# Performance work log

Measured on AMD Instinct MI355X. Metric: run time of the kernel, lower is better.

Reference implementation:

```python
import jax, jax.numpy as jnp
import numpy as np

L, N, D = 4, 50000, 64        # lookback, n_nodes, gnn_dim
E = 500000                    # n_edges
HID = 256
LN_EPS = 1e-5


def setup_inputs() -> dict:
    key = jax.random.key(0)
    ks = jax.random.split(key, 8)
    h_all = jax.random.normal(ks[0], (L, N, D), dtype=jnp.float32)
    src = jax.random.randint(ks[1], (E,), 0, N, dtype=jnp.int32)
    dst = jax.random.randint(ks[2], (E,), 0, N, dtype=jnp.int32)
    W1 = jax.random.normal(ks[3], (HID, L * 2 * D), dtype=jnp.float32) * (1.0 / np.sqrt(L * 2 * D))
    b1 = jax.random.normal(ks[4], (HID,), dtype=jnp.float32) * 0.01
    W3 = jax.random.normal(ks[5], (1, HID), dtype=jnp.float32) * (1.0 / np.sqrt(HID))
    b3 = jax.random.normal(ks[6], (1,), dtype=jnp.float32) * 0.01
    gamma2 = jnp.ones((HID,), dtype=jnp.float32)
    beta2 = jnp.zeros((HID,), dtype=jnp.float32)
    return {"h_all": h_all, "src": src, "dst": dst, "W1": W1, "b1": b1,
            "W3": W3, "b3": b3, "gamma2": gamma2, "beta2": beta2}


def reference(h_all, src, dst, W1, b1, W3, b3, gamma2, beta2):
    lb, _, d = h_all.shape
    # importance weights 1..L normalized
    imp = jnp.arange(1, lb + 1, dtype=h_all.dtype)
    imp = imp / imp.sum()
    # per-edge gather of src/dst features for every lookback step: [L, E, 2D]
    hs = h_all[:, src]                                  # [L, E, D]
    hd = h_all[:, dst]                                  # [L, E, D]
    embed = jnp.concatenate([hs, hd], axis=-1) * imp[:, None, None]
    # concat over lookback steps -> [E, L*2D]
    embed = jnp.transpose(embed, (1, 0, 2)).reshape(embed.shape[1], -1)
    # MLP: W1(tanh) -> LayerNorm -> dropout(eval=identity) -> relu -> W3
    x = jnp.tanh(embed) @ W1.T + b1                     # [E, HID]
    mu = jnp.mean(x, axis=-1, keepdims=True)
    var = jnp.var(x, axis=-1, keepdims=True)
    x = (x - mu) * jax.lax.rsqrt(var + LN_EPS) * gamma2 + beta2
    x = jax.nn.relu(x)
    out = x @ W3.T + b3                                 # [E, 1]
    return out[:, 0]
```

## Files before the change

### kernel.cpp

```cpp
#include <hip/hip_runtime.h>
#include <hip/hip_bf16.h>

#define LL 4
#define NN 50000
#define DD 64
#define EE 500000
#define HID 256
#define KDIM 512
#define LN_EPS 1e-5f

typedef __bf16 bf16x8 __attribute__((ext_vector_type(8)));
typedef float f32x16 __attribute__((ext_vector_type(16)));

__device__ __forceinline__ void async16(const void* g, void* l) {
    __builtin_amdgcn_global_load_lds(
        (const __attribute__((address_space(1))) void*)g,
        (__attribute__((address_space(3))) void*)l, 16, 0, 0);
}

__global__ void tanh_conv(const float* __restrict__ h, __bf16* __restrict__ t) {
    int i = (blockIdx.x * 256 + threadIdx.x) * 8;
    int l = i / (NN * DD);
    float imp = (float)(l + 1) * 0.1f;
    const float4* p = (const float4*)(h + i);
    float4 a = p[0];
    float4 b = p[1];
    float x[8] = {a.x, a.y, a.z, a.w, b.x, b.y, b.z, b.w};
    bf16x8 r;
    #pragma unroll
    for (int j = 0; j < 8; ++j) {
        float e2 = __expf(2.0f * (imp * x[j]));
        r[j] = (__bf16)(1.0f - 2.0f / (e2 + 1.0f));
    }
    *(bf16x8*)(t + i) = r;
}

__global__ void w2_conv(const float* __restrict__ w1, __bf16* __restrict__ o) {
    int t = blockIdx.x * 256 + threadIdx.x;
    int j  = t & 511;
    int b  = t >> 9;
    int k0 = (b >> 1) * 16 + (b & 1) * 8;
    int r  = j & 255;
    int col = (k0 >> 6) * 128 + ((j >> 8) ? 64 : 0) + (k0 & 63);
    const float4* p = (const float4*)(w1 + r * KDIM + col);
    float4 va = p[0];
    float4 vb = p[1];
    bf16x8 v;
    v[0] = (__bf16)va.x; v[1] = (__bf16)va.y; v[2] = (__bf16)va.z; v[3] = (__bf16)va.w;
    v[4] = (__bf16)vb.x; v[5] = (__bf16)vb.y; v[6] = (__bf16)vb.z; v[7] = (__bf16)vb.w;
    *(bf16x8*)(o + (size_t)t * 8) = v;
}

__global__ __launch_bounds__(256, 2)
void node_proj(const __bf16* __restrict__ tb, const __bf16* __restrict__ w2c,
               const float* __restrict__ b1, __bf16* __restrict__ P) {
    __shared__ __align__(16) char smem[65536];
    __bf16* Bs = (__bf16*)smem;
    float*  Cs = (float*)smem;

    const int tid  = threadIdx.x;
    const int wave = tid >> 6;
    const int lane = tid & 63;
    const int h32  = lane >> 5;
    const int c32  = lane & 31;
    const int cb   = blockIdx.y;
    const int n00  = blockIdx.x * 128;

    #pragma unroll
    for (int it = 0; it < 16; ++it) {
        int o = it * 2048 + tid * 8;
        async16(w2c + (size_t)(o >> 10) * 4096 + cb * 1024 + (o & 1023), Bs + o);
    }

    float badd[8];
    {
        int c0 = (tid * 8) & 127;
        if (cb >= 2) {
            const float4* pb = (const float4*)(b1 + (cb - 2) * 128 + c0);
            float4 u = pb[0], v = pb[1];
            badd[0] = u.x; badd[1] = u.y; badd[2] = u.z; badd[3] = u.w;
            badd[4] = v.x; badd[5] = v.y; badd[6] = v.z; badd[7] = v.w;
        } else {
            #pragma unroll
            for (int z = 0; z < 8; ++z) badd[z] = 0.f;
        }
    }

    int node = n00 + wave * 32 + c32;
    if (node >= NN) node = NN - 1;
    uint4 a[16];
    #pragma unroll
    for (int u = 0; u < 16; ++u) {
        const __bf16* p = tb + (size_t)(u >> 2) * (NN * DD) + node * DD
                        + (u & 3) * 16 + h32 * 8;
        a[u] = *(const uint4*)p;
    }

    f32x16 acc[4];
    #pragma unroll
    for (int nt = 0; nt < 4; ++nt) acc[nt] = (f32x16)(0.f);

    __syncthreads();

    #pragma unroll
    for (int u = 0; u < 16; ++u) {
        bf16x8 af = __builtin_bit_cast(bf16x8, a[u]);
        const __bf16* Bk = Bs + (u * 2 + h32) * 1024 + c32 * 8;
        #pragma unroll
        for (int nt = 0; nt < 4; ++nt) {
            bf16x8 bf = *(const bf16x8*)(Bk + nt * 256);
            acc[nt] = __builtin_amdgcn_mfma_f32_32x32x16_bf16(af, bf, acc[nt], 0, 0, 0);
        }
    }
    __syncthreads();

    #pragma unroll
    for (int nt = 0; nt < 4; ++nt) {
        #pragma unroll
        for (int r = 0; r < 16; ++r) {
            int nl = wave * 32 + (r & 3) + 8 * (r >> 2) + 4 * h32;
            Cs[nl * 128 + nt * 32 + c32] = acc[nt][r];
        }
    }
    __syncthreads();
    #pragma unroll
    for (int it = 0; it < 8; ++it) {
        int o  = it * 2048 + tid * 8;
        int nl = o >> 7;
        int n  = n00 + nl;
        if (n < NN) {
            bf16x8 v;
            #pragma unroll
            for (int z = 0; z < 8; ++z) v[z] = (__bf16)(Cs[o + z] + badd[z]);
            *(bf16x8*)(P + (size_t)n * 512 + cb * 128 + (o & 127)) = v;
        }
    }
}

__global__ __launch_bounds__(256, 3)
void edge_out(const __bf16* __restrict__ P, const int* __restrict__ src,
              const int* __restrict__ dst,
              const float* __restrict__ w3, const float* __restrict__ b3,
              const float* __restrict__ gamma, const float* __restrict__ beta,
              float* __restrict__ out) {
    const int tid = threadIdx.x;
    const int g   = tid >> 4;
    const int j   = tid & 15;

    float gv[16], btv[16], wv[16];
    {
        const float4* pg = (const float4*)(gamma + j * 16);
        const float4* pt = (const float4*)(beta + j * 16);
        const float4* pw = (const float4*)(w3 + j * 16);
        #pragma unroll
        for (int z = 0; z < 4; ++z) {
            float4 vg = pg[z], vt = pt[z], vw = pw[z];
            gv [z*4+0] = vg.x; gv [z*4+1] = vg.y; gv [z*4+2] = vg.z; gv [z*4+3] = vg.w;
            btv[z*4+0] = vt.x; btv[z*4+1] = vt.y; btv[z*4+2] = vt.z; btv[z*4+3] = vt.w;
            wv [z*4+0] = vw.x; wv [z*4+1] = vw.y; wv [z*4+2] = vw.z; wv [z*4+3] = vw.w;
        }
    }
    const float b3v = b3[0];
    const int e0 = blockIdx.x * 128 + g * 8;

    int ep = e0 + (j & 7);
    if (ep >= EE) ep = EE - 1;
    const int sj = src[ep];
    const int dj = dst[ep];

    uint4 s0[3], s1[3], d0[3], d1[3];

    #pragma unroll
    for (int i = 0; i < 2; ++i) {
        int s = __shfl(sj, i, 16);
        int d = __shfl(dj, i, 16);
        const uint4* ps = (const uint4*)(P + (size_t)s * 512 + j * 16);
        const uint4* pd = (const uint4*)(P + (size_t)d * 512 + 256 + j * 16);
        s0[i] = ps[0]; s1[i] = ps[1]; d0[i] = pd[0]; d1[i] = pd[1];
    }

    #pragma unroll
    for (int i = 0; i < 8; ++i) {
        if (i + 2 < 8) {
            const int slot = (i + 2) % 3;
            int s = __shfl(sj, i + 2, 16);
            int d = __shfl(dj, i + 2, 16);
            const uint4* ps = (const uint4*)(P + (size_t)s * 512 + j * 16);
            const uint4* pd = (const uint4*)(P + (size_t)d * 512 + 256 + j * 16);
            s0[slot] = ps[0]; s1[slot] = ps[1]; d0[slot] = pd[0]; d1[slot] = pd[1];
        }
        const int cs = i % 3;
        bf16x8 a0 = __builtin_bit_cast(bf16x8, s0[cs]);
        bf16x8 a1 = __builtin_bit_cast(bf16x8, s1[cs]);
        bf16x8 c0 = __builtin_bit_cast(bf16x8, d0[cs]);
        bf16x8 c1 = __builtin_bit_cast(bf16x8, d1[cs]);
        float x[16];
        #pragma unroll
        for (int z = 0; z < 8; ++z) {
            x[z]     = (float)a0[z] + (float)c0[z];
            x[z + 8] = (float)a1[z] + (float)c1[z];
        }
        float sum = 0.f, sq = 0.f;
        #pragma unroll
        for (int z = 0; z < 16; ++z) {
            sum += x[z];
            sq   = fmaf(x[z], x[z], sq);
        }
        #pragma unroll
        for (int m = 1; m < 16; m <<= 1) {
            sum += __shfl_xor(sum, m);
            sq  += __shfl_xor(sq,  m);
        }
        float mu = sum * (1.0f / 256.0f);
        float rs = rsqrtf(sq * (1.0f / 256.0f) - mu * mu + LN_EPS);
        float dot = 0.f;
        #pragma unroll
        for (int z = 0; z < 16; ++z) {
            float y = fmaxf((x[z] - mu) * rs * gv[z] + btv[z], 0.f);
            dot = fmaf(y, wv[z], dot);
        }
        #pragma unroll
        for (int m = 1; m < 16; m <<= 1) dot += __shfl_xor(dot, m);
        int e = e0 + i;
        if (j == 0 && e < EE) out[e] = dot + b3v;
    }

    #pragma unroll
    for (int z = 0; z < 16; ++z)
        asm volatile("" :: "v"(gv[z]), "v"(btv[z]), "v"(wv[z]));
}

extern "C" void kernel_launch(void* const* d_in, const int* in_sizes, int n_in,
                              void* d_out, int out_size, void* d_ws, size_t ws_size,
                              hipStream_t stream) {
    const float* h_all  = (const float*)d_in[0];
    const int*   src    = (const int*)  d_in[1];
    const int*   dst    = (const int*)  d_in[2];
    const float* W1     = (const float*)d_in[3];
    const float* b1     = (const float*)d_in[4];
    const float* W3     = (const float*)d_in[5];
    const float* b3     = (const float*)d_in[6];
    const float* gamma2 = (const float*)d_in[7];
    const float* beta2  = (const float*)d_in[8];
    float* out = (float*)d_out;

    __bf16* tb  = (__bf16*)d_ws;
    __bf16* w2c = tb + (size_t)LL * NN * DD;
    __bf16* P   = w2c + 131072;

    tanh_conv<<<6250, 256, 0, stream>>>(h_all, tb);
    w2_conv<<<64, 256, 0, stream>>>(W1, w2c);
    node_proj<<<dim3((NN + 127) / 128, 4), 256, 0, stream>>>(tb, w2c, b1, P);
    edge_out<<<(EE + 127) / 128, 256, 0, stream>>>(P, src, dst, W3, b3,
                                                   gamma2, beta2, out);
}
```

Measured before the change: 201.7 us.

## Fuse tanh conversion into node projection and loop over column chunks in-block

Drops the separate tanh/bf16 conversion kernel and computes tanh(imp*h) directly from fp32 inputs inside the node projection, so the intermediate bf16 tensor is never written and re-read. Each block now handles all 512 output columns for its 128 nodes, streaming the weight chunks through a double-buffered LDS tile with async loads. Results are written straight from the accumulators with scattered per-element bf16 stores instead of an LDS-staged coalesced store. This trades one fewer launch and less DRAM traffic for a serial column loop per block, fewer blocks, and poorly coalesced output writes.

```diff
diff --git a/kernel.cpp b/kernel.cpp
--- a/kernel.cpp
+++ b/kernel.cpp
@@ -16,23 +16,6 @@
     __builtin_amdgcn_global_load_lds(
         (const __attribute__((address_space(1))) void*)g,
         (__attribute__((address_space(3))) void*)l, 16, 0, 0);
-}
-
-__global__ void tanh_conv(const float* __restrict__ h, __bf16* __restrict__ t) {
-    int i = (blockIdx.x * 256 + threadIdx.x) * 8;
-    int l = i / (NN * DD);
-    float imp = (float)(l + 1) * 0.1f;
-    const float4* p = (const float4*)(h + i);
-    float4 a = p[0];
-    float4 b = p[1];
-    float x[8] = {a.x, a.y, a.z, a.w, b.x, b.y, b.z, b.w};
-    bf16x8 r;
-    #pragma unroll
-    for (int j = 0; j < 8; ++j) {
-        float e2 = __expf(2.0f * (imp * x[j]));
-        r[j] = (__bf16)(1.0f - 2.0f / (e2 + 1.0f));
-    }
-    *(bf16x8*)(t + i) = r;
 }
 
 __global__ void w2_conv(const float* __restrict__ w1, __bf16* __restrict__ o) {
@@ -51,89 +34,83 @@
     *(bf16x8*)(o + (size_t)t * 8) = v;
 }
 
-__global__ __launch_bounds__(256, 2)
-void node_proj(const __bf16* __restrict__ tb, const __bf16* __restrict__ w2c,
+__global__ __launch_bounds__(256, 4)
+void node_proj(const float* __restrict__ h, const __bf16* __restrict__ w2c,
                const float* __restrict__ b1, __bf16* __restrict__ P) {
-    __shared__ __align__(16) char smem[65536];
-    __bf16* Bs = (__bf16*)smem;
-    float*  Cs = (float*)smem;
+    __shared__ __align__(16) __bf16 Bs[2][16384];
 
     const int tid  = threadIdx.x;
     const int wave = tid >> 6;
     const int lane = tid & 63;
     const int h32  = lane >> 5;
     const int c32  = lane & 31;
-    const int cb   = blockIdx.y;
     const int n00  = blockIdx.x * 128;
 
     #pragma unroll
-    for (int it = 0; it < 16; ++it) {
+    for (int it = 0; it < 8; ++it) {
         int o = it * 2048 + tid * 8;
-        async16(w2c + (size_t)(o >> 10) * 4096 + cb * 1024 + (o & 1023), Bs + o);
-    }
-
-    float badd[8];
-    {
-        int c0 = (tid * 8) & 127;
-        if (cb >= 2) {
-            const float4* pb = (const float4*)(b1 + (cb - 2) * 128 + c0);
-            float4 u = pb[0], v = pb[1];
-            badd[0] = u.x; badd[1] = u.y; badd[2] = u.z; badd[3] = u.w;
-            badd[4] = v.x; badd[5] = v.y; badd[6] = v.z; badd[7] = v.w;
-        } else {
-            #pragma unroll
-            for (int z = 0; z < 8; ++z) badd[z] = 0.f;
-        }
+        async16(w2c + (size_t)(o >> 9) * 4096 + (o & 511), &Bs[0][o]);
     }
 
     int node = n00 + wave * 32 + c32;
     if (node >= NN) node = NN - 1;
-    uint4 a[16];
+    bf16x8 af[16];
     #pragma unroll
     for (int u = 0; u < 16; ++u) {
-        const __bf16* p = tb + (size_t)(u >> 2) * (NN * DD) + node * DD
-                        + (u & 3) * 16 + h32 * 8;
-        a[u] = *(const uint4*)p;
-    }
-
-    f32x16 acc[4];
-    #pragma unroll
-    for (int nt = 0; nt < 4; ++nt) acc[nt] = (f32x16)(0.f);
+        int l = u >> 2;
+        float imp = (float)(l + 1) * 0.1f;
+        const float* p = h + (size_t)l * (NN * DD) + node * DD
+                       + (u & 3) * 16 + h32 * 8;
+        float4 va = *(const float4*)p;
+        float4 vb = *(const float4*)(p + 4);
+        float xv[8] = {va.x, va.y, va.z, va.w, vb.x, vb.y, vb.z, vb.w};
+        #pragma unroll
+        for (int z = 0; z < 8; ++z) {
+            float e2 = __expf(2.0f * (imp * xv[z]));
+            af[u][z] = (__bf16)(1.0f - 2.0f / (e2 + 1.0f));
+        }
+    }
 
     __syncthreads();
 
-    #pragma unroll
-    for (int u = 0; u < 16; ++u) {
-        bf16x8 af = __builtin_bit_cast(bf16x8, a[u]);
-        const __bf16* Bk = Bs + (u * 2 + h32) * 1024 + c32 * 8;
-        #pragma unroll
-        for (int nt = 0; nt < 4; ++nt) {
-            bf16x8 bf = *(const bf16x8*)(Bk + nt * 256);
-            acc[nt] = __builtin_amdgcn_mfma_f32_32x32x16_bf16(af, bf, acc[nt], 0, 0, 0);
-        }
-    }
-    __syncthreads();
-
-    #pragma unroll
-    for (int nt = 0; nt < 4; ++nt) {
-        #pragma unroll
-        for (int r = 0; r < 16; ++r) {
-            int nl = wave * 32 + (r & 3) + 8 * (r >> 2) + 4 * h32;
-            Cs[nl * 128 + nt * 32 + c32] = acc[nt][r];
-        }
-    }
-    __syncthreads();
-    #pragma unroll
-    for (int it = 0; it < 8; ++it) {
-        int o  = it * 2048 + tid * 8;
-        int nl = o >> 7;
-        int n  = n00 + nl;
-        if (n < NN) {
-            bf16x8 v;
+    for (int p = 0; p < 8; ++p) {
+        const int bp = p & 1;
+        if (p < 7) {
             #pragma unroll
-            for (int z = 0; z < 8; ++z) v[z] = (__bf16)(Cs[o + z] + badd[z]);
-            *(bf16x8*)(P + (size_t)n * 512 + cb * 128 + (o & 127)) = v;
-        }
+            for (int it = 0; it < 8; ++it) {
+                int o = it * 2048 + tid * 8;
+                async16(w2c + (size_t)(o >> 9) * 4096 + (p + 1) * 512 + (o & 511),
+                        &Bs[bp ^ 1][o]);
+            }
+        }
+
+        f32x16 acc[2];
+        acc[0] = (f32x16)(0.f);
+        acc[1] = (f32x16)(0.f);
+        #pragma unroll
+        for (int u = 0; u < 16; ++u) {
+            const __bf16* Bk = &Bs[bp][(u * 2 + h32) * 512 + c32 * 8];
+            #pragma unroll
+            for (int nt = 0; nt < 2; ++nt) {
+                bf16x8 bf = *(const bf16x8*)(Bk + nt * 256);
+                acc[nt] = __builtin_amdgcn_mfma_f32_32x32x16_bf16(af[u], bf, acc[nt], 0, 0, 0);
+            }
+        }
+
+        #pragma unroll
+        for (int nt = 0; nt < 2; ++nt) {
+            int col = p * 64 + nt * 32 + c32;
+            float b1v = (col >= 256) ? b1[col - 256] : 0.f;
+            #pragma unroll
+            for (int r = 0; r < 16; ++r) {
+                int row = (r & 3) + 8 * (r >> 2) + 4 * h32;
+                int n = n00 + wave * 32 + row;
+                if (n < NN)
+                    P[(size_t)n * 512 + col] = (__bf16)(acc[nt][r] + b1v);
+            }
+        }
+
+        __syncthreads();
     }
 }
 
@@ -223,6 +200,7 @@
         for (int m = 1; m < 16; m <<= 1) dot += __shfl_xor(dot, m);
         int e = e0 + i;
         if (j == 0 && e < EE) out[e] = dot + b3v;
+        cs0: ;
     }
 
     #pragma unroll
@@ -244,13 +222,11 @@
     const float* beta2  = (const float*)d_in[8];
     float* out = (float*)d_out;
 
-    __bf16* tb  = (__bf16*)d_ws;
-    __bf16* w2c = tb + (size_t)LL * NN * DD;
+    __bf16* w2c = (__bf16*)d_ws;
     __bf16* P   = w2c + 131072;
 
-    tanh_conv<<<6250, 256, 0, stream>>>(h_all, tb);
     w2_conv<<<64, 256, 0, stream>>>(W1, w2c);
-    node_proj<<<dim3((NN + 127) / 128, 4), 256, 0, stream>>>(tb, w2c, b1, P);
+    node_proj<<<(NN + 127) / 128, 256, 0, stream>>>(h_all, w2c, b1, P);
     edge_out<<<(EE + 127) / 128, 256, 0, stream>>>(P, src, dst, W3, b3,
                                                    gamma2, beta2, out);
 }
```

Result: slower. 216.7 us (+7.5%).
